# Kernel tuning notes

Measured on AMD Instinct MI355X. Metric: run time of the kernel, lower is better.

The kernel has to match this reference:

```python
import jax, jax.numpy as jnp
import numpy as np

# Production-scale dims (see shape_source)
N = 100_000      # total nodes (tokens)
E = 1_600_000    # edges
B = 2_000        # graphs / documents
VOCAB = 50_000
NW = 256         # word_vec width == GraphConv out channels (args.nw)
ENC = 512        # args.enc_nh
K = 100          # args.num_topic
EPS = 1e-5       # BatchNorm eps


def setup_inputs() -> dict:
    key = jax.random.key(0)
    ks = jax.random.split(key, 24)
    idx_x = jax.random.randint(ks[0], (N,), 0, VOCAB)
    idx_w = jnp.ones((1,), jnp.float32)          # scalar self-loop weight
    x_batch = jnp.sort(jax.random.randint(ks[1], (N,), 0, B))
    edge_index = jax.random.randint(ks[2], (2, E), 0, N)
    edge_weight = jax.random.uniform(ks[3], (E,), jnp.float32)
    # Parameters
    s = 0.02
    word_vec = jax.random.normal(ks[4], (VOCAB, NW), jnp.float32) * s
    Wrel = jax.random.normal(ks[5], (NW, NW), jnp.float32) * s   # GraphConv lin_rel
    brel = jnp.zeros((NW,), jnp.float32)
    Wroot = jax.random.normal(ks[6], (NW, NW), jnp.float32) * s  # GraphConv lin_root (no bias)
    bn_gamma = jnp.ones((NW,), jnp.float32)
    bn_beta = jnp.zeros((NW,), jnp.float32)
    W1 = jax.random.normal(ks[7], (ENC, 2 * NW), jnp.float32) * s  # enc2_fc1
    b1 = jnp.zeros((ENC,), jnp.float32)
    W2 = jax.random.normal(ks[8], (ENC, 2 * NW), jnp.float32) * s  # enc2_fc2
    b2 = jnp.zeros((ENC,), jnp.float32)
    Wm = jax.random.normal(ks[9], (K, ENC), jnp.float32) * s       # mean_fc
    bm = jnp.zeros((K,), jnp.float32)
    Wv = jnp.zeros((K, ENC), jnp.float32)                          # logvar_fc zero-init
    bv = jnp.zeros((K,), jnp.float32)
    Wphi = jax.random.normal(ks[10], (K, 2 * NW + ENC), jnp.float32) * s  # phi_fc
    bphi = jnp.zeros((K,), jnp.float32)
    return dict(idx_x=idx_x, idx_w=idx_w, x_batch=x_batch, edge_index=edge_index,
                edge_weight=edge_weight, word_vec=word_vec, Wrel=Wrel, brel=brel,
                Wroot=Wroot, bn_gamma=bn_gamma, bn_beta=bn_beta, W1=W1, b1=b1,
                W2=W2, b2=b2, Wm=Wm, bm=bm, Wv=Wv, bv=bv, Wphi=Wphi, bphi=bphi)


def reference(idx_x, idx_w, x_batch, edge_index, edge_weight, word_vec,
              Wrel, brel, Wroot, bn_gamma, bn_beta, W1, b1, W2, b2,
              Wm, bm, Wv, bv, Wphi, bphi):
    # Embedding gather
    x = word_vec[idx_x]                                # [N, NW]
    src, dst = edge_index[0], edge_index[1]
    # GraphConv with explicit self-loops of weight idx_w (diag edges in original)
    msg = edge_weight[:, None] * x[src]                # [E, NW]
    aggr = jax.ops.segment_sum(msg, dst, num_segments=N) + idx_w * x
    h = aggr @ Wrel.T + brel + x @ Wroot.T             # lin_rel(aggr) + lin_root(x)
    # BatchNorm1d (training-mode batch stats, biased variance) + tanh
    mu = jnp.mean(h, axis=0)
    var = jnp.mean((h - mu) ** 2, axis=0)
    enc1 = jnp.tanh((h - mu) * jax.lax.rsqrt(var + EPS) * bn_gamma + bn_beta)
    enc1 = jnp.concatenate([enc1, x], axis=-1)         # [N, 2*NW]
    # GLU gate
    enc2 = jax.nn.sigmoid(enc1 @ W1.T + b1) * jnp.tanh(enc1 @ W2.T + b2)  # [N, ENC]
    # Scatter-sum pooling per document (dropout is identity in eval)
    pooled = jax.ops.segment_sum(enc2, x_batch, num_segments=B)            # [B, ENC]
    mean = pooled @ Wm.T + bm                          # [B, K]
    logvar = pooled @ Wv.T + bv                        # [B, K]
    # Gather re-expansion + softmax
    word_embed = jnp.concatenate([enc1, pooled[x_batch]], axis=-1)         # [N, 2*NW+ENC]
    phi = jax.nn.softmax(word_embed @ Wphi.T + bphi, axis=-1)              # [N, K]
    return mean, logvar, phi
```

## Files before the change

### kernel.cpp

```cpp
#include <hip/hip_runtime.h>
#include <hip/hip_bf16.h>

#define NW 256
#define D2 512
#define PK 1024
#define BM 128
#define BK 64
#define DPB 8

typedef unsigned short u16;
typedef short bf16x8 __attribute__((ext_vector_type(8)));
typedef float f32x4 __attribute__((ext_vector_type(4)));

__device__ __forceinline__ float bf2f(u16 u) {
    union { unsigned u; float f; } v; v.u = ((unsigned)u) << 16; return v.f;
}
__device__ __forceinline__ u16 f2bf(float f) {
    union { float f; unsigned u; } v; v.f = f;
    unsigned u = v.u;
    return (u16)((u + 0x7fffu + ((u >> 16) & 1u)) >> 16);
}
__device__ __forceinline__ float tanh_fast(float x) {
    return 1.f - 2.f / (1.f + __expf(2.f * x));
}

__device__ __forceinline__ void stage_tile(const u16* __restrict__ base, int row0, int maxrow,
                                           int ldk, int k0, u16* lds, int tid) {
    int w = tid >> 6, l = tid & 63;
#pragma unroll
    for (int i = 0; i < 4; ++i) {
        int loadIdx = i * 256 + w * 64 + l;
        int row = loadIdx >> 3, s = loadIdx & 7;
        int srow = row0 + row; if (srow > maxrow) srow = maxrow;
        int scol = k0 + ((s ^ (row & 7)) << 3);
        const u16* g = base + (size_t)srow * ldk + scol;
        u16* ld = lds + (size_t)(i * 256 + w * 64) * 8;
        __builtin_amdgcn_global_load_lds((const __attribute__((address_space(1))) void*)g,
                                         (__attribute__((address_space(3))) void*)ld, 16, 0, 0);
    }
}

__device__ __forceinline__ bf16x8 lds_frag(const u16* lds, int row, int kc, int g) {
    int byte = (row << 7) + (kc << 6) + (g << 4);
    byte ^= (row & 7) << 4;
    return *(const bf16x8*)((const char*)lds + byte);
}

__global__ void k_wcat(const float* __restrict__ Wrel, const float* __restrict__ Wroot,
                       u16* __restrict__ wcat) {
    int i = blockIdx.x * blockDim.x + threadIdx.x;
    if (i < NW * D2) {
        int c = i >> 9, k = i & 511;
        float v = (k < NW) ? Wrel[c * NW + k] : Wroot[c * NW + (k - NW)];
        wcat[i] = f2bf(v);
    }
}
__global__ void k_wpair(const float* __restrict__ W1, const float* __restrict__ W2,
                        u16* __restrict__ wp) {
    int i = blockIdx.x * blockDim.x + threadIdx.x;
    if (i < 1024 * 512) {
        int row = i >> 9, k = i & 511;
        int c = row >> 7, j = row & 127;
        float v = (j < 64) ? W1[(size_t)(c * 64 + j) * D2 + k]
                           : W2[(size_t)(c * 64 + j - 64) * D2 + k];
        wp[i] = f2bf(v);
    }
}
__global__ void k_wphi(const float* __restrict__ Wphi, u16* __restrict__ wp, int K) {
    int i = blockIdx.x * blockDim.x + threadIdx.x;
    if (i < 128 * 1024) {
        int r = i >> 10, k = i & 1023;
        wp[i] = f2bf(r < K ? Wphi[(size_t)r * PK + k] : 0.f);
    }
}

__global__ void k_gather(const int* __restrict__ idx, const float* __restrict__ wv,
                         u16* __restrict__ X, int N) {
    int row = blockIdx.x * 4 + (threadIdx.x >> 6);
    int lane = threadIdx.x & 63;
    if (row < N) {
        int id = idx[row];
        float4 v = *(const float4*)(wv + (size_t)id * NW + lane * 4);
        ushort4 o;
        o.x = f2bf(v.x); o.y = f2bf(v.y); o.z = f2bf(v.z); o.w = f2bf(v.w);
        *(ushort4*)(X + (size_t)row * D2 + NW + lane * 4) = o;
    }
}

__global__ void k_hist(const int* __restrict__ ei, int* __restrict__ deg, int E) {
    int e = blockIdx.x * blockDim.x + threadIdx.x;
    if (e < E) atomicAdd(&deg[ei[E + e]], 1);
}
__global__ __launch_bounds__(1024) void k_scan(const int* __restrict__ deg,
                                               int* __restrict__ rowptr, int N) {
    const int T = 1024;
    int t = threadIdx.x;
    int chunk = (N + T - 1) / T;
    int beg = t * chunk, end = min(beg + chunk, N);
    int s = 0;
    for (int i = beg; i < end; ++i) s += deg[i];
    __shared__ int ls[T];
    ls[t] = s; __syncthreads();
    for (int d = 1; d < T; d <<= 1) {
        int v = (t >= d) ? ls[t - d] : 0;
        __syncthreads();
        ls[t] += v;
        __syncthreads();
    }
    int run = ls[t] - s;
    for (int i = beg; i < end; ++i) { rowptr[i] = run; run += deg[i]; }
    if (t == T - 1) rowptr[N] = run;
}
__global__ void k_scatter(const int* __restrict__ ei, const float* __restrict__ ew,
                          const int* __restrict__ rowptr, int* __restrict__ cursor,
                          int* __restrict__ ecols, float* __restrict__ evals, int E) {
    int e = blockIdx.x * blockDim.x + threadIdx.x;
    if (e < E) {
        int d = ei[E + e];
        int p = rowptr[d] + atomicAdd(&cursor[d], 1);
        ecols[p] = ei[e];
        evals[p] = ew[e];
    }
}

__global__ void k_spmm(const int* __restrict__ rowptr, const int* __restrict__ ecols,
                       const float* __restrict__ evals, const float* __restrict__ idxw,
                       u16* __restrict__ X, int N) {
    int n = blockIdx.x * 4 + (threadIdx.x >> 6);
    int l = threadIdx.x & 63;
    if (n >= N) return;
    int half = l >> 5, li = l & 31;
    float a[8];
    bf16x8 xv = *(const bf16x8*)(X + (size_t)n * D2 + NW + li * 8);
    float iw = idxw[0];
#pragma unroll
    for (int j = 0; j < 8; ++j) a[j] = half ? 0.f : iw * bf2f((u16)xv[j]);
    int r0 = rowptr[n], r1 = rowptr[n + 1];
#pragma unroll 4
    for (int e = r0 + half; e < r1; e += 2) {
        int s = ecols[e];
        float w = evals[e];
        bf16x8 v = *(const bf16x8*)(X + (size_t)s * D2 + NW + li * 8);
#pragma unroll
        for (int j = 0; j < 8; ++j) a[j] += w * bf2f((u16)v[j]);
    }
#pragma unroll
    for (int j = 0; j < 8; ++j) a[j] += __shfl_xor(a[j], 32);
    if (half == 0) {
        bf16x8 o;
#pragma unroll
        for (int j = 0; j < 8; ++j) o[j] = (short)f2bf(a[j]);
        *(bf16x8*)(X + (size_t)n * D2 + li * 8) = o;
    }
}

__global__ __launch_bounds__(256) void k_gemm_h(const u16* __restrict__ A, const u16* __restrict__ W,
                                                const float* __restrict__ brel, u16* __restrict__ H,
                                                float* __restrict__ sums, float* __restrict__ sumsq,
                                                int M, int MT) {
    int b = blockIdx.x;
    int xcd = b & 7, j = b >> 3;
    int chunk = j & 1;
    int panel = (j >> 1) * 8 + xcd;
    if (panel >= MT) return;
    __shared__ u16 As[2][BM * BK], Ws[2][BM * BK];
    int tid = threadIdx.x;
    int w = tid >> 6, l = tid & 63, l16 = l & 15, g = l >> 4;
    int row0 = panel * BM;
    const u16* wbase = W + (size_t)chunk * 128 * D2;
    f32x4 acc[2][8];
#pragma unroll
    for (int m = 0; m < 2; ++m)
#pragma unroll
        for (int n = 0; n < 8; ++n) { f32x4 z = {0.f, 0.f, 0.f, 0.f}; acc[m][n] = z; }

    stage_tile(A, row0, M - 1, D2, 0, As[0], tid);
    stage_tile(wbase, 0, 127, D2, 0, Ws[0], tid);
    __syncthreads();
    int buf = 0;
    for (int kt = 0; kt < 8; ++kt) {
        if (kt < 7) {
            stage_tile(A, row0, M - 1, D2, (kt + 1) * BK, As[buf ^ 1], tid);
            stage_tile(wbase, 0, 127, D2, (kt + 1) * BK, Ws[buf ^ 1], tid);
        }
#pragma unroll
        for (int kc = 0; kc < 2; ++kc) {
            bf16x8 a0 = lds_frag(As[buf], w * 32 + l16, kc, g);
            bf16x8 a1 = lds_frag(As[buf], w * 32 + 16 + l16, kc, g);
#pragma unroll
            for (int n = 0; n < 8; ++n) {
                bf16x8 bb = lds_frag(Ws[buf], n * 16 + l16, kc, g);
                acc[0][n] = __builtin_amdgcn_mfma_f32_16x16x32_bf16(a0, bb, acc[0][n], 0, 0, 0);
                acc[1][n] = __builtin_amdgcn_mfma_f32_16x16x32_bf16(a1, bb, acc[1][n], 0, 0, 0);
            }
        }
        __syncthreads();
        buf ^= 1;
    }
    float* ssum = (float*)As[0];
    float* ssq  = ssum + 128;
    if (tid < 128) { ssum[tid] = 0.f; ssq[tid] = 0.f; }
    __syncthreads();
    int colb = chunk * 128;
#pragma unroll
    for (int n = 0; n < 8; ++n) {
        int lcol = n * 16 + l16;
        int col = colb + lcol;
        float bb = brel[col];
        float cs = 0.f, cq = 0.f;
#pragma unroll
        for (int m = 0; m < 2; ++m) {
            int row = row0 + w * 32 + m * 16 + g * 4;
#pragma unroll
            for (int r = 0; r < 4; ++r) {
                if (row + r < M) {
                    float v = acc[m][n][r] + bb;
                    H[(size_t)(row + r) * NW + col] = f2bf(v);
                    cs += v; cq += v * v;
                }
            }
        }
        cs += __shfl_xor(cs, 16); cs += __shfl_xor(cs, 32);
        cq += __shfl_xor(cq, 16); cq += __shfl_xor(cq, 32);
        if (g == 0) { atomicAdd(&ssum[lcol], cs); atomicAdd(&ssq[lcol], cq); }
    }
    __syncthreads();
    if (tid < 128) {
        atomicAdd(&sums[colb + tid], ssum[tid]);
        atomicAdd(&sumsq[colb + tid], ssq[tid]);
    }
}

__global__ void k_bnprep(const float* __restrict__ sums, const float* __restrict__ sumsq,
                         const float* __restrict__ gamma, const float* __restrict__ beta,
                         float* __restrict__ bnab, int N) {
    int c = threadIdx.x;
    float inv = 1.f / (float)N;
    float mu = sums[c] * inv;
    float var = sumsq[c] * inv - mu * mu;
    float rs = rsqrtf(var + 1e-5f);
    float a = rs * gamma[c];
    bnab[c] = a;
    bnab[NW + c] = beta[c] - mu * a;
}

__global__ void k_enc1(const u16* __restrict__ H, const float* __restrict__ bnab,
                       u16* __restrict__ X, int N) {
    int row = blockIdx.x * 4 + (threadIdx.x >> 6);
    int lane = threadIdx.x & 63;
    if (row >= N) return;
    int c = lane * 4;
    ushort4 hv = *(const ushort4*)(H + (size_t)row * NW + c);
    ushort4 o;
    o.x = f2bf(tanh_fast(bf2f(hv.x) * bnab[c + 0] + bnab[NW + c + 0]));
    o.y = f2bf(tanh_fast(bf2f(hv.y) * bnab[c + 1] + bnab[NW + c + 1]));
    o.z = f2bf(tanh_fast(bf2f(hv.z) * bnab[c + 2] + bnab[NW + c + 2]));
    o.w = f2bf(tanh_fast(bf2f(hv.w) * bnab[c + 3] + bnab[NW + c + 3]));
    *(ushort4*)(X + (size_t)row * D2 + c) = o;
}

__global__ __launch_bounds__(256) void k_glu(const u16* __restrict__ A, const u16* __restrict__ Wp,
                                             const float* __restrict__ b1, const float* __restrict__ b2,
                                             u16* __restrict__ enc2, int M, int MT) {
    int b = blockIdx.x;
    int xcd = b & 7, j = b >> 3;
    int chunk = j & 7;
    int panel = (j >> 3) * 8 + xcd;
    if (panel >= MT) return;
    __shared__ u16 As[2][BM * BK], Ws[2][BM * BK];
    int tid = threadIdx.x;
    int w = tid >> 6, l = tid & 63, l16 = l & 15, g = l >> 4;
    int row0 = panel * BM;
    const u16* wbase = Wp + (size_t)chunk * 128 * D2;
    f32x4 acc[2][8];
#pragma unroll
    for (int m = 0; m < 2; ++m)
#pragma unroll
        for (int n = 0; n < 8; ++n) { f32x4 z = {0.f, 0.f, 0.f, 0.f}; acc[m][n] = z; }

    stage_tile(A, row0, M - 1, D2, 0, As[0], tid);
    stage_tile(wbase, 0, 127, D2, 0, Ws[0], tid);
    __syncthreads();
    int buf = 0;
    for (int kt = 0; kt < 8; ++kt) {
        if (kt < 7) {
            stage_tile(A, row0, M - 1, D2, (kt + 1) * BK, As[buf ^ 1], tid);
            stage_tile(wbase, 0, 127, D2, (kt + 1) * BK, Ws[buf ^ 1], tid);
        }
#pragma unroll
        for (int kc = 0; kc < 2; ++kc) {
            bf16x8 a0 = lds_frag(As[buf], w * 32 + l16, kc, g);
            bf16x8 a1 = lds_frag(As[buf], w * 32 + 16 + l16, kc, g);
#pragma unroll
            for (int n = 0; n < 8; ++n) {
                bf16x8 bb = lds_frag(Ws[buf], n * 16 + l16, kc, g);
                acc[0][n] = __builtin_amdgcn_mfma_f32_16x16x32_bf16(a0, bb, acc[0][n], 0, 0, 0);
                acc[1][n] = __builtin_amdgcn_mfma_f32_16x16x32_bf16(a1, bb, acc[1][n], 0, 0, 0);
            }
        }
        __syncthreads();
        buf ^= 1;
    }
    int colb = chunk * 64;
#pragma unroll
    for (int m = 0; m < 2; ++m) {
        int row = row0 + w * 32 + m * 16 + g * 4;
#pragma unroll
        for (int n = 0; n < 4; ++n) {
            int col = colb + n * 16 + l16;
            float f1 = b1[col], f2 = b2[col];
#pragma unroll
            for (int r = 0; r < 4; ++r) {
                if (row + r < M) {
                    float g1 = acc[m][n][r] + f1;
                    float g2 = acc[m][n + 4][r] + f2;
                    float sg = 1.f / (1.f + __expf(-g1));
                    enc2[(size_t)(row + r) * D2 + col] = f2bf(sg * tanh_fast(g2));
                }
            }
        }
    }
}

__global__ void k_docptr(const int* __restrict__ xb, int* __restrict__ dp, int N, int B) {
    int b = blockIdx.x * blockDim.x + threadIdx.x;
    if (b <= B) {
        int lo = 0, hi = N;
        while (lo < hi) { int mid = (lo + hi) >> 1; if (xb[mid] < b) lo = mid + 1; else hi = mid; }
        dp[b] = lo;
    }
}

__global__ void k_pool(const u16* __restrict__ enc2, const int* __restrict__ dp,
                       float* __restrict__ pooled, u16* __restrict__ pooledb, int B) {
    int b = blockIdx.x, t = threadIdx.x;
    int r0 = dp[b], r1 = dp[b + 1];
    float a0 = 0.f, a1 = 0.f;
    for (int r = r0; r < r1; ++r) {
        a0 += bf2f(enc2[(size_t)r * D2 + t]);
        a1 += bf2f(enc2[(size_t)r * D2 + 256 + t]);
    }
    pooled[(size_t)b * D2 + t] = a0;
    pooled[(size_t)b * D2 + 256 + t] = a1;
    pooledb[(size_t)b * D2 + t] = f2bf(a0);
    pooledb[(size_t)b * D2 + 256 + t] = f2bf(a1);
}

__global__ __launch_bounds__(128) void k_meanvar(const float* __restrict__ pooled,
                                                 const float* __restrict__ Wm,
                                                 const float* __restrict__ bm,
                                                 const float* __restrict__ Wv,
                                                 const float* __restrict__ bv,
                                                 float* __restrict__ out, int B, int K) {
    __shared__ float sp[DPB][D2];
    int b0 = blockIdx.x * DPB;
    int t = threadIdx.x;
    for (int i = t; i < DPB * D2; i += 128) {
        int d = i >> 9, c = i & 511;
        int b = b0 + d;
        sp[d][c] = (b < B) ? pooled[(size_t)b * D2 + c] : 0.f;
    }
    __syncthreads();
    if (t < K) {
        float m[DPB], v[DPB];
#pragma unroll
        for (int d = 0; d < DPB; ++d) { m[d] = 0.f; v[d] = 0.f; }
        const float* wm = Wm + (size_t)t * D2;
        const float* wv = Wv + (size_t)t * D2;
        for (int c = 0; c < D2; ++c) {
            float a = wm[c], bb = wv[c];
#pragma unroll
            for (int d = 0; d < DPB; ++d) {
                m[d] += sp[d][c] * a;
                v[d] += sp[d][c] * bb;
            }
        }
        float mb = bm[t], vb = bv[t];
#pragma unroll
        for (int d = 0; d < DPB; ++d) {
            int b = b0 + d;
            if (b < B) {
                out[(size_t)b * K + t] = m[d] + mb;
                out[(size_t)B * K + (size_t)b * K + t] = v[d] + vb;
            }
        }
    }
}

__device__ __forceinline__ void stage_phiA(const u16* __restrict__ X, const u16* __restrict__ PB,
                                           const int* __restrict__ xb, int row0, int M,
                                           int k0, u16* lds, int tid) {
    int w = tid >> 6, l = tid & 63;
#pragma unroll
    for (int i = 0; i < 4; ++i) {
        int loadIdx = i * 256 + w * 64 + l;
        int row = loadIdx >> 3, s = loadIdx & 7;
        int srow = row0 + row; if (srow >= M) srow = M - 1;
        int scol = k0 + ((s ^ (row & 7)) << 3);
        const u16* gsrc = (scol < D2) ? X + (size_t)srow * D2 + scol
                                      : PB + (size_t)xb[srow] * D2 + (scol - D2);
        u16* ld = lds + (size_t)(i * 256 + w * 64) * 8;
        __builtin_amdgcn_global_load_lds((const __attribute__((address_space(1))) void*)gsrc,
                                         (__attribute__((address_space(3))) void*)ld, 16, 0, 0);
    }
}

__global__ __launch_bounds__(256) void k_phi(const u16* __restrict__ X, const u16* __restrict__ PB,
                                             const int* __restrict__ xb, const u16* __restrict__ Wp,
                                             const float* __restrict__ bphi, float* __restrict__ out,
                                             int M, int B, int K) {
    __shared__ u16 As[2][BM * BK], Ws[2][BM * BK];
    int tid = threadIdx.x;
    int w = tid >> 6, l = tid & 63, l16 = l & 15, g = l >> 4;
    int row0 = blockIdx.x * BM;
    f32x4 acc[2][8];
#pragma unroll
    for (int m = 0; m < 2; ++m)
#pragma unroll
        for (int n = 0; n < 8; ++n) { f32x4 z = {0.f, 0.f, 0.f, 0.f}; acc[m][n] = z; }

    stage_phiA(X, PB, xb, row0, M, 0, As[0], tid);
    stage_tile(Wp, 0, 127, PK, 0, Ws[0], tid);
    __syncthreads();
    int buf = 0;
    for (int kt = 0; kt < 16; ++kt) {
        if (kt < 15) {
            stage_phiA(X, PB, xb, row0, M, (kt + 1) * BK, As[buf ^ 1], tid);
            stage_tile(Wp, 0, 127, PK, (kt + 1) * BK, Ws[buf ^ 1], tid);
        }
#pragma unroll
        for (int kc = 0; kc < 2; ++kc) {
            bf16x8 a0 = lds_frag(As[buf], w * 32 + l16, kc, g);
            bf16x8 a1 = lds_frag(As[buf], w * 32 + 16 + l16, kc, g);
#pragma unroll
            for (int n = 0; n < 8; ++n) {
                bf16x8 bb = lds_frag(Ws[buf], n * 16 + l16, kc, g);
                acc[0][n] = __builtin_amdgcn_mfma_f32_16x16x32_bf16(a0, bb, acc[0][n], 0, 0, 0);
                acc[1][n] = __builtin_amdgcn_mfma_f32_16x16x32_bf16(a1, bb, acc[1][n], 0, 0, 0);
            }
        }
        __syncthreads();
        buf ^= 1;
    }
    size_t outoff = (size_t)2 * B * K;
#pragma unroll
    for (int m = 0; m < 2; ++m) {
        int rb = row0 + w * 32 + m * 16 + g * 4;
#pragma unroll
        for (int r = 0; r < 4; ++r) {
            int row = rb + r;
            if (row >= M) continue;
            float v[7];
            float mx = -1e30f;
#pragma unroll
            for (int n = 0; n < 7; ++n) {
                int col = n * 16 + l16;
                float t = (col < K) ? acc[m][n][r] + bphi[col] : -1e30f;
                v[n] = t;
                mx = fmaxf(mx, t);
            }
            mx = fmaxf(mx, __shfl_xor(mx, 1));
            mx = fmaxf(mx, __shfl_xor(mx, 2));
            mx = fmaxf(mx, __shfl_xor(mx, 4));
            mx = fmaxf(mx, __shfl_xor(mx, 8));
            float s = 0.f;
#pragma unroll
            for (int n = 0; n < 7; ++n) {
                int col = n * 16 + l16;
                float e = (col < K) ? __expf(v[n] - mx) : 0.f;
                v[n] = e;
                s += e;
            }
            s += __shfl_xor(s, 1);
            s += __shfl_xor(s, 2);
            s += __shfl_xor(s, 4);
            s += __shfl_xor(s, 8);
            float inv = 1.f / s;
#pragma unroll
            for (int n = 0; n < 7; ++n) {
                int col = n * 16 + l16;
                if (col < K) out[outoff + (size_t)row * K + col] = v[n] * inv;
            }
        }
    }
}

extern "C" void kernel_launch(void* const* d_in, const int* in_sizes, int n_in,
                              void* d_out, int out_size, void* d_ws, size_t ws_size,
                              hipStream_t stream) {
    const int N = in_sizes[0];
    const int E = in_sizes[4];
    const int K = in_sizes[16];
    const int B = (int)(((size_t)out_size - (size_t)N * K) / (2 * (size_t)K));

    const int*   idx_x   = (const int*)d_in[0];
    const float* idx_w   = (const float*)d_in[1];
    const int*   x_batch = (const int*)d_in[2];
    const int*   ei      = (const int*)d_in[3];
    const float* ew      = (const float*)d_in[4];
    const float* word_vec= (const float*)d_in[5];
    const float* Wrel    = (const float*)d_in[6];
    const float* brel    = (const float*)d_in[7];
    const float* Wroot   = (const float*)d_in[8];
    const float* gamma   = (const float*)d_in[9];
    const float* beta    = (const float*)d_in[10];
    const float* W1      = (const float*)d_in[11];
    const float* b1      = (const float*)d_in[12];
    const float* W2      = (const float*)d_in[13];
    const float* b2      = (const float*)d_in[14];
    const float* Wm      = (const float*)d_in[15];
    const float* bm      = (const float*)d_in[16];
    const float* Wv      = (const float*)d_in[17];
    const float* bv      = (const float*)d_in[18];
    const float* Wphi    = (const float*)d_in[19];
    const float* bphi    = (const float*)d_in[20];
    float* out = (float*)d_out;

    char* p = (char*)d_ws;
    auto take = [&](size_t bytes) -> char* {
        char* r = p;
        p += (bytes + 255) & ~(size_t)255;
        return r;
    };
    u16* X = (u16*)take((size_t)N * D2 * 2);
    char* Ybase = take((size_t)N * D2 * 2);
    u16*   hb   = (u16*)Ybase;
    u16*   enc2 = (u16*)Ybase;
    char* q = Ybase;
    auto takeY = [&](size_t bytes) -> char* {
        char* r = q;
        q += (bytes + 255) & ~(size_t)255;
        return r;
    };
    int*   rowptr = (int*)takeY((size_t)(N + 1) * 4);
    int*   cursor = (int*)takeY((size_t)N * 4);
    int*   ecols  = (int*)takeY((size_t)E * 4);
    float* evals  = (float*)takeY((size_t)E * 4);
    u16*   wcat    = (u16*)take((size_t)NW * D2 * 2);
    u16*   wglu    = (u16*)take((size_t)1024 * D2 * 2);
    u16*   wphib   = (u16*)take((size_t)128 * PK * 2);
    int*   docptr  = (int*)take((size_t)(B + 1) * 4);
    float* pooled  = (float*)take((size_t)B * D2 * 4);
    u16*   pooledb = (u16*)take((size_t)B * D2 * 2);
    float* sums    = (float*)take(NW * 4);
    float* sumsq   = (float*)take(NW * 4);
    float* bnab    = (float*)take(2 * NW * 4);

    if ((size_t)(p - (char*)d_ws) > ws_size) return;

    hipMemsetAsync(cursor, 0, (size_t)N * 4, stream);
    hipMemsetAsync(sums, 0, NW * 4, stream);
    hipMemsetAsync(sumsq, 0, NW * 4, stream);

    k_wcat<<<(NW * D2 + 255) / 256, 256, 0, stream>>>(Wrel, Wroot, wcat);
    k_wpair<<<(1024 * D2 + 255) / 256, 256, 0, stream>>>(W1, W2, wglu);
    k_wphi<<<(128 * PK + 255) / 256, 256, 0, stream>>>(Wphi, wphib, K);

    k_gather<<<(N + 3) / 4, 256, 0, stream>>>(idx_x, word_vec, X, N);
    k_hist<<<(E + 255) / 256, 256, 0, stream>>>(ei, cursor, E);
    k_scan<<<1, 1024, 0, stream>>>(cursor, rowptr, N);
    hipMemsetAsync(cursor, 0, (size_t)N * 4, stream);
    k_scatter<<<(E + 255) / 256, 256, 0, stream>>>(ei, ew, rowptr, cursor, ecols, evals, E);
    k_spmm<<<(N + 3) / 4, 256, 0, stream>>>(rowptr, ecols, evals, idx_w, X, N);

    int MT = (N + BM - 1) / BM;
    int P8 = (MT + 7) / 8;
    k_gemm_h<<<P8 * 8 * 2, 256, 0, stream>>>(X, wcat, brel, hb, sums, sumsq, N, MT);
    k_bnprep<<<1, NW, 0, stream>>>(sums, sumsq, gamma, beta, bnab, N);
    k_enc1<<<(N + 3) / 4, 256, 0, stream>>>(hb, bnab, X, N);

    k_glu<<<P8 * 8 * 8, 256, 0, stream>>>(X, wglu, b1, b2, enc2, N, MT);

    k_docptr<<<(B + 1 + 255) / 256, 256, 0, stream>>>(x_batch, docptr, N, B);
    k_pool<<<B, 256, 0, stream>>>(enc2, docptr, pooled, pooledb, B);
    k_meanvar<<<(B + DPB - 1) / DPB, 128, 0, stream>>>(pooled, Wm, bm, Wv, bv, out, B, K);
    k_phi<<<MT, 256, 0, stream>>>(X, pooledb, x_batch, wphib, bphi, out, N, B, K);
}
```

Baseline: 949.2 us.

## Fuse document pooling into GLU GEMM epilogue via atomics; merge weight prep kernels

```diff
diff --git a/kernel.cpp b/kernel.cpp
--- a/kernel.cpp
+++ b/kernel.cpp
@@ -46,32 +46,30 @@
     return *(const bf16x8*)((const char*)lds + byte);
 }
 
-__global__ void k_wcat(const float* __restrict__ Wrel, const float* __restrict__ Wroot,
-                       u16* __restrict__ wcat) {
+__global__ void k_wprep(const float* __restrict__ Wrel, const float* __restrict__ Wroot,
+                        const float* __restrict__ W1, const float* __restrict__ W2,
+                        const float* __restrict__ Wphi,
+                        u16* __restrict__ wcat, u16* __restrict__ wglu,
+                        u16* __restrict__ wphib, float* __restrict__ sums,
+                        float* __restrict__ sumsq, int K) {
     int i = blockIdx.x * blockDim.x + threadIdx.x;
     if (i < NW * D2) {
         int c = i >> 9, k = i & 511;
         float v = (k < NW) ? Wrel[c * NW + k] : Wroot[c * NW + (k - NW)];
         wcat[i] = f2bf(v);
     }
-}
-__global__ void k_wpair(const float* __restrict__ W1, const float* __restrict__ W2,
-                        u16* __restrict__ wp) {
-    int i = blockIdx.x * blockDim.x + threadIdx.x;
     if (i < 1024 * 512) {
         int row = i >> 9, k = i & 511;
         int c = row >> 7, j = row & 127;
         float v = (j < 64) ? W1[(size_t)(c * 64 + j) * D2 + k]
                            : W2[(size_t)(c * 64 + j - 64) * D2 + k];
-        wp[i] = f2bf(v);
-    }
-}
-__global__ void k_wphi(const float* __restrict__ Wphi, u16* __restrict__ wp, int K) {
-    int i = blockIdx.x * blockDim.x + threadIdx.x;
+        wglu[i] = f2bf(v);
+    }
     if (i < 128 * 1024) {
         int r = i >> 10, k = i & 1023;
-        wp[i] = f2bf(r < K ? Wphi[(size_t)r * PK + k] : 0.f);
-    }
+        wphib[i] = f2bf(r < K ? Wphi[(size_t)r * PK + k] : 0.f);
+    }
+    if (i < NW) { sums[i] = 0.f; sumsq[i] = 0.f; }
 }
 
 __global__ void k_gather(const int* __restrict__ idx, const float* __restrict__ wv,
@@ -91,7 +89,7 @@
     int e = blockIdx.x * blockDim.x + threadIdx.x;
     if (e < E) atomicAdd(&deg[ei[E + e]], 1);
 }
-__global__ __launch_bounds__(1024) void k_scan(const int* __restrict__ deg,
+__global__ __launch_bounds__(1024) void k_scan(int* __restrict__ deg,
                                                int* __restrict__ rowptr, int N) {
     const int T = 1024;
     int t = threadIdx.x;
@@ -108,7 +106,12 @@
         __syncthreads();
     }
     int run = ls[t] - s;
-    for (int i = beg; i < end; ++i) { rowptr[i] = run; run += deg[i]; }
+    for (int i = beg; i < end; ++i) {
+        int d = deg[i];
+        rowptr[i] = run;
+        run += d;
+        deg[i] = 0;
+    }
     if (t == T - 1) rowptr[N] = run;
 }
 __global__ void k_scatter(const int* __restrict__ ei, const float* __restrict__ ew,
@@ -261,7 +264,8 @@
 
 __global__ __launch_bounds__(256) void k_glu(const u16* __restrict__ A, const u16* __restrict__ Wp,
                                              const float* __restrict__ b1, const float* __restrict__ b2,
-                                             u16* __restrict__ enc2, int M, int MT) {
+                                             const int* __restrict__ xb, float* __restrict__ pooled,
+                                             int M, int MT) {
     int b = blockIdx.x;
     int xcd = b & 7, j = b >> 3;
     int chunk = j & 7;
@@ -301,49 +305,50 @@
         __syncthreads();
         buf ^= 1;
     }
+    int drow[2][4];
+#pragma unroll
+    for (int m = 0; m < 2; ++m) {
+        int rowb = row0 + w * 32 + m * 16 + g * 4;
+#pragma unroll
+        for (int r = 0; r < 4; ++r)
+            drow[m][r] = (rowb + r < M) ? xb[rowb + r] : -1;
+    }
     int colb = chunk * 64;
 #pragma unroll
-    for (int m = 0; m < 2; ++m) {
-        int row = row0 + w * 32 + m * 16 + g * 4;
-#pragma unroll
-        for (int n = 0; n < 4; ++n) {
-            int col = colb + n * 16 + l16;
-            float f1 = b1[col], f2 = b2[col];
+    for (int n = 0; n < 4; ++n) {
+        int col = colb + n * 16 + l16;
+        float f1 = b1[col], f2 = b2[col];
+#pragma unroll
+        for (int m = 0; m < 2; ++m) {
+            int dcur = -1;
+            float run = 0.f;
 #pragma unroll
             for (int r = 0; r < 4; ++r) {
-                if (row + r < M) {
+                int d = drow[m][r];
+                if (d >= 0) {
                     float g1 = acc[m][n][r] + f1;
                     float g2 = acc[m][n + 4][r] + f2;
-                    float sg = 1.f / (1.f + __expf(-g1));
-                    enc2[(size_t)(row + r) * D2 + col] = f2bf(sg * tanh_fast(g2));
+                    float v = (1.f / (1.f + __expf(-g1))) * tanh_fast(g2);
+                    if (d != dcur) {
+                        if (dcur >= 0) atomicAdd(&pooled[(size_t)dcur * D2 + col], run);
+                        dcur = d; run = 0.f;
+                    }
+                    run += v;
                 }
             }
-        }
-    }
-}
-
-__global__ void k_docptr(const int* __restrict__ xb, int* __restrict__ dp, int N, int B) {
-    int b = blockIdx.x * blockDim.x + threadIdx.x;
-    if (b <= B) {
-        int lo = 0, hi = N;
-        while (lo < hi) { int mid = (lo + hi) >> 1; if (xb[mid] < b) lo = mid + 1; else hi = mid; }
-        dp[b] = lo;
-    }
-}
-
-__global__ void k_pool(const u16* __restrict__ enc2, const int* __restrict__ dp,
-                       float* __restrict__ pooled, u16* __restrict__ pooledb, int B) {
-    int b = blockIdx.x, t = threadIdx.x;
-    int r0 = dp[b], r1 = dp[b + 1];
-    float a0 = 0.f, a1 = 0.f;
-    for (int r = r0; r < r1; ++r) {
-        a0 += bf2f(enc2[(size_t)r * D2 + t]);
-        a1 += bf2f(enc2[(size_t)r * D2 + 256 + t]);
-    }
-    pooled[(size_t)b * D2 + t] = a0;
-    pooled[(size_t)b * D2 + 256 + t] = a1;
-    pooledb[(size_t)b * D2 + t] = f2bf(a0);
-    pooledb[(size_t)b * D2 + 256 + t] = f2bf(a1);
+            if (dcur >= 0) atomicAdd(&pooled[(size_t)dcur * D2 + col], run);
+        }
+    }
+}
+
+__global__ void k_p2b(const float* __restrict__ pooled, u16* __restrict__ pooledb, int n4) {
+    int i = blockIdx.x * blockDim.x + threadIdx.x;
+    if (i < n4) {
+        float4 v = *(const float4*)(pooled + (size_t)i * 4);
+        ushort4 o;
+        o.x = f2bf(v.x); o.y = f2bf(v.y); o.z = f2bf(v.z); o.w = f2bf(v.w);
+        *(ushort4*)(pooledb + (size_t)i * 4) = o;
+    }
 }
 
 __global__ __launch_bounds__(128) void k_meanvar(const float* __restrict__ pooled,
@@ -525,7 +530,6 @@
     u16* X = (u16*)take((size_t)N * D2 * 2);
     char* Ybase = take((size_t)N * D2 * 2);
     u16*   hb   = (u16*)Ybase;
-    u16*   enc2 = (u16*)Ybase;
     char* q = Ybase;
     auto takeY = [&](size_t bytes) -> char* {
         char* r = q;
@@ -539,7 +543,6 @@
     u16*   wcat    = (u16*)take((size_t)NW * D2 * 2);
     u16*   wglu    = (u16*)take((size_t)1024 * D2 * 2);
     u16*   wphib   = (u16*)take((size_t)128 * PK * 2);
-    int*   docptr  = (int*)take((size_t)(B + 1) * 4);
     float* pooled  = (float*)take((size_t)B * D2 * 4);
     u16*   pooledb = (u16*)take((size_t)B * D2 * 2);
     float* sums    = (float*)take(NW * 4);
@@ -549,17 +552,14 @@
     if ((size_t)(p - (char*)d_ws) > ws_size) return;
 
     hipMemsetAsync(cursor, 0, (size_t)N * 4, stream);
-    hipMemsetAsync(sums, 0, NW * 4, stream);
-    hipMemsetAsync(sumsq, 0, NW * 4, stream);
-
-    k_wcat<<<(NW * D2 + 255) / 256, 256, 0, stream>>>(Wrel, Wroot, wcat);
-    k_wpair<<<(1024 * D2 + 255) / 256, 256, 0, stream>>>(W1, W2, wglu);
-    k_wphi<<<(128 * PK + 255) / 256, 256, 0, stream>>>(Wphi, wphib, K);
+    hipMemsetAsync(pooled, 0, (size_t)B * D2 * 4, stream);
+
+    k_wprep<<<(1024 * 512 + 255) / 256, 256, 0, stream>>>(Wrel, Wroot, W1, W2, Wphi,
+                                                          wcat, wglu, wphib, sums, sumsq, K);
 
     k_gather<<<(N + 3) / 4, 256, 0, stream>>>(idx_x, word_vec, X, N);
     k_hist<<<(E + 255) / 256, 256, 0, stream>>>(ei, cursor, E);
     k_scan<<<1, 1024, 0, stream>>>(cursor, rowptr, N);
-    hipMemsetAsync(cursor, 0, (size_t)N * 4, stream);
     k_scatter<<<(E + 255) / 256, 256, 0, stream>>>(ei, ew, rowptr, cursor, ecols, evals, E);
     k_spmm<<<(N + 3) / 4, 256, 0, stream>>>(rowptr, ecols, evals, idx_w, X, N);
 
@@ -569,10 +569,10 @@
     k_bnprep<<<1, NW, 0, stream>>>(sums, sumsq, gamma, beta, bnab, N);
     k_enc1<<<(N + 3) / 4, 256, 0, stream>>>(hb, bnab, X, N);
 
-    k_glu<<<P8 * 8 * 8, 256, 0, stream>>>(X, wglu, b1, b2, enc2, N, MT);
-
-    k_docptr<<<(B + 1 + 255) / 256, 256, 0, stream>>>(x_batch, docptr, N, B);
-    k_pool<<<B, 256, 0, stream>>>(enc2, docptr, pooled, pooledb, B);
+    k_glu<<<P8 * 8 * 8, 256, 0, stream>>>(X, wglu, b1, b2, x_batch, pooled, N, MT);
+
+    int n4 = (B * D2) / 4;
+    k_p2b<<<(n4 + 255) / 256, 256, 0, stream>>>(pooled, pooledb, n4);
     k_meanvar<<<(B + DPB - 1) / DPB, 128, 0, stream>>>(pooled, Wm, bm, Wv, bv, out, B, K);
     k_phi<<<MT, 256, 0, stream>>>(X, pooledb, x_batch, wphib, bphi, out, N, B, K);
 }
```

Measured after the change: 1.004 ms. 1.06x slower.
